# Performance work log

Hardware: AMD Instinct MI355X
Metric: run time of the kernel (lower is better)

## Reference

```python
import jax, jax.numpy as jnp
import numpy as np

B = 32768
H = W = 5          # grid_size
NC = 4             # num_colors
E = 64             # embed_dim
HID = 128          # hidden_dim
OUT = 128          # output_dim
NH = 4             # num_heads
HD = E // NH       # head_dim = 16


def _lin(k, fan_in, fan_out):
    w = jax.random.normal(k, (fan_in, fan_out), jnp.float32) / np.sqrt(fan_in)
    b = jnp.zeros((fan_out,), jnp.float32)
    return w, b


def setup_inputs() -> dict:
    key = jax.random.key(0)
    ks = jax.random.split(key, 16)
    obs = jax.random.randint(ks[0], (B, 3, H, W), 0, NC, dtype=jnp.int32)
    color_embed = jax.random.normal(ks[1], (NC, E), jnp.float32)
    row_embed = jax.random.normal(ks[2], (H, E // 2), jnp.float32)
    col_embed = jax.random.normal(ks[3], (W, E // 2), jnp.float32)
    ip_w1, ip_b1 = _lin(ks[4], 2 * E, HID)
    ip_w2, ip_b2 = _lin(ks[5], HID, E)
    q_w, q_b = _lin(ks[6], E, E)
    k_w, k_b = _lin(ks[7], E, E)
    v_w, v_b = _lin(ks[8], E, E)
    o_w, o_b = _lin(ks[9], E, E)
    op_w1, op_b1 = _lin(ks[10], 2 * E, HID)
    op_w2, op_b2 = _lin(ks[11], HID, E)
    cb_w1, cb_b1 = _lin(ks[12], 3 * E, HID)
    cb_w2, cb_b2 = _lin(ks[13], HID, OUT)
    return dict(obs=obs, color_embed=color_embed, row_embed=row_embed, col_embed=col_embed,
                ip_w1=ip_w1, ip_b1=ip_b1, ip_w2=ip_w2, ip_b2=ip_b2,
                q_w=q_w, q_b=q_b, k_w=k_w, k_b=k_b, v_w=v_w, v_b=v_b, o_w=o_w, o_b=o_b,
                op_w1=op_w1, op_b1=op_b1, op_w2=op_w2, op_b2=op_b2,
                cb_w1=cb_w1, cb_b1=cb_b1, cb_w2=cb_w2, cb_b2=cb_b2)


def _mlp(x, w1, b1, w2, b2):
    return jax.nn.relu(x @ w1 + b1) @ w2 + b2


def reference(obs, color_embed, row_embed, col_embed,
              ip_w1, ip_b1, ip_w2, ip_b2,
              q_w, q_b, k_w, k_b, v_w, v_b, o_w, o_b,
              op_w1, op_b1, op_w2, op_b2,
              cb_w1, cb_b1, cb_w2, cb_b2):
    Bn = obs.shape[0]
    input_grid, output_grid, mask = obs[:, 0], obs[:, 1], obs[:, 2]

    # 2D learned positional embedding: concat(row_emb[i], col_emb[j]) -> [H, W, E]
    pos = jnp.concatenate([
        jnp.broadcast_to(row_embed[:, None, :], (H, W, E // 2)),
        jnp.broadcast_to(col_embed[None, :, :], (H, W, E // 2))], axis=-1)
    pos_b = jnp.broadcast_to(pos, (Bn, H, W, E))

    # input branch: color embed + pos -> MLP -> [B, H*W, E]
    in_feat = jnp.concatenate([color_embed[input_grid], pos_b], axis=-1)
    inp_flat = _mlp(in_feat, ip_w1, ip_b1, ip_w2, ip_b2).reshape(Bn, H * W, E)

    # first nonzero mask position per batch (row-major), zero embedding if none
    mflat = (mask != 0).reshape(Bn, H * W)
    has = jnp.any(mflat, axis=1)
    idx = jnp.argmax(mflat, axis=1)
    r, c = idx // W, idx % W
    cpe = jnp.where(has[:, None],
                    jnp.concatenate([row_embed[r], col_embed[c]], axis=-1),
                    0.0)  # [B, E]

    # single-query cross-attention over the 25 input cells
    q = (cpe @ q_w + q_b).reshape(Bn, NH, HD)
    k = (inp_flat @ k_w + k_b).reshape(Bn, H * W, NH, HD)
    v = (inp_flat @ v_w + v_b).reshape(Bn, H * W, NH, HD)
    attn = jax.nn.softmax(jnp.einsum('bhd,bkhd->bhk', q, k) * (HD ** -0.5), axis=-1)
    attended = jnp.einsum('bhk,bkhd->bhd', attn, v).reshape(Bn, E) @ o_w + o_b

    # output branch: MLP then mean-pool over grid
    out_feat = jnp.concatenate([color_embed[output_grid], pos_b], axis=-1)
    out_ctx = _mlp(out_feat, op_w1, op_b1, op_w2, op_b2).mean(axis=(1, 2))

    combined = jnp.concatenate([attended, out_ctx, cpe], axis=-1)  # [B, 3E]
    return _mlp(combined, cb_w1, cb_b1, cb_w2, cb_b2)  # [B, OUT]
```

## Files before the change

kernel.cpp:

```cpp
#include <hip/hip_runtime.h>
#include <hip/hip_bf16.h>


typedef __attribute__((ext_vector_type(8))) short short8v;
typedef __attribute__((ext_vector_type(4))) float float4v;

static __device__ __forceinline__ short f2bfs(float f) {
  __hip_bfloat16 h = __float2bfloat16(f);
  return *reinterpret_cast<short*>(&h);
}
static __device__ __forceinline__ float bfs2f(short s) {
  return __uint_as_float(((unsigned)(unsigned short)s) << 16);
}
static __device__ __forceinline__ unsigned short f2bf(float f) {
  unsigned int u = __float_as_uint(f);
  unsigned int r = (u + 0x7fffu + ((u >> 16) & 1u)) >> 16;
  return (unsigned short)r;
}

__global__ __launch_bounds__(128) void prepE(
    const float* __restrict__ color_embed, const float* __restrict__ row_embed,
    const float* __restrict__ col_embed,
    const float* __restrict__ ip_w1, const float* __restrict__ ip_b1,
    const float* __restrict__ ip_w2, const float* __restrict__ ip_b2,
    const float* __restrict__ op_w1, const float* __restrict__ op_b1,
    const float* __restrict__ op_w2, const float* __restrict__ op_b2,
    const float* __restrict__ q_w, const float* __restrict__ q_b,
    const float* __restrict__ o_w, const float* __restrict__ o_b,
    const float* __restrict__ cb_w1, const float* __restrict__ cb_b1,
    const float* __restrict__ cb_w2,
    float* __restrict__ inpval, float* __restrict__ outval,
    float* __restrict__ qtab, float* __restrict__ cpeproj,
    float* __restrict__ bias1,
    unsigned short* __restrict__ wovT, unsigned short* __restrict__ cbw2T) {
  const int bid = blockIdx.x, t = threadIdx.x;
  if (bid < 200) {
    __shared__ float feat[128];
    __shared__ float h1[128];
    const int path = bid / 100;
    const int cij = bid % 100;
    const int c = cij / 25, ij = cij % 25, gi = ij / 5, gj = ij % 5;
    if (t < 64)      feat[t] = color_embed[c * 64 + t];
    else if (t < 96) feat[t] = row_embed[gi * 32 + (t - 64)];
    else             feat[t] = col_embed[gj * 32 + (t - 96)];
    __syncthreads();
    const float* w1 = path ? op_w1 : ip_w1;
    const float* b1 = path ? op_b1 : ip_b1;
    float acc = b1[t];
#pragma unroll 8
    for (int d = 0; d < 128; ++d) acc = fmaf(feat[d], w1[d * 128 + t], acc);
    h1[t] = fmaxf(acc, 0.f);
    __syncthreads();
    if (t < 64) {
      const float* w2 = path ? op_w2 : ip_w2;
      const float* b2 = path ? op_b2 : ip_b2;
      float v = b2[t];
#pragma unroll 8
      for (int d = 0; d < 128; ++d) v = fmaf(h1[d], w2[d * 64 + t], v);
      (path ? outval : inpval)[cij * 64 + t] = v;
    }
    return;
  }
  const int fid = (bid - 200) * 128 + t;
  if (fid < 1664) {
    const int p = fid >> 6, e2 = fid & 63;
    float a = q_b[e2];
    if (p < 25) {
      const int r = p / 5, cc = p % 5;
#pragma unroll 8
      for (int e = 0; e < 32; ++e) a = fmaf(row_embed[r * 32 + e], q_w[e * 64 + e2], a);
#pragma unroll 8
      for (int e = 0; e < 32; ++e) a = fmaf(col_embed[cc * 32 + e], q_w[(32 + e) * 64 + e2], a);
    }
    qtab[fid] = a;
  } else if (fid < 4992) {
    const int l = fid - 1664;
    const int p = l >> 7, jj = l & 127;
    float a = 0.f;
    if (p < 25) {
      const int r = p / 5, cc = p % 5;
#pragma unroll 8
      for (int e = 0; e < 32; ++e) a = fmaf(row_embed[r * 32 + e], cb_w1[(128 + e) * 128 + jj], a);
#pragma unroll 8
      for (int e = 0; e < 32; ++e) a = fmaf(col_embed[cc * 32 + e], cb_w1[(160 + e) * 128 + jj], a);
    }
    cpeproj[l] = a;
  } else if (fid < 5120) {
    const int jj = fid - 4992;
    float a = cb_b1[jj];
#pragma unroll 8
    for (int e = 0; e < 64; ++e) a = fmaf(o_b[e], cb_w1[e * 128 + jj], a);
    bias1[jj] = a;
  } else if (fid < 13312) {
    const int i = fid - 5120;
    const int col = i >> 6, d = i & 63;
    float a = 0.f;
#pragma unroll 8
    for (int e = 0; e < 64; ++e) a = fmaf(o_w[d * 64 + e], cb_w1[e * 128 + col], a);
    wovT[i] = f2bf(a);
  } else if (fid < 29696) {
    const int i = fid - 13312;
    const int col = i >> 7, k = i & 127;
    cbw2T[i] = f2bf(cb_w2[k * 128 + col]);
  }
}

__global__ __launch_bounds__(256) void prepF(
    const float* __restrict__ k_w, const float* __restrict__ k_b,
    const float* __restrict__ v_w, const float* __restrict__ v_b,
    const float* __restrict__ cb_w1,
    const float* __restrict__ qtab, const float* __restrict__ cpeproj,
    const float* __restrict__ bias1,
    const float* __restrict__ inpval, const float* __restrict__ outval,
    float* __restrict__ stab, unsigned short* __restrict__ vtabT,
    unsigned short* __restrict__ outprojBT) {
  const int bid = blockIdx.x, t = threadIdx.x;
  if (bid < 100) {
    __shared__ float kk[64];
    const int ig = bid / 25, ij = bid % 25;
    const float* x = inpval + bid * 64;
    if (t < 64) {
      float a = k_b[t];
#pragma unroll 8
      for (int e = 0; e < 64; ++e) a = fmaf(x[e], k_w[e * 64 + t], a);
      kk[t] = a;
    } else if (t < 128) {
      const int e2 = t - 64;
      float a = v_b[e2];
#pragma unroll 8
      for (int e = 0; e < 64; ++e) a = fmaf(x[e], v_w[e * 64 + e2], a);
      vtabT[(e2 >> 4) * 2048 + (e2 & 15) * 128 + 4 * ij + ig] = f2bf(a);
    } else {
      const int col = t - 128;
      const float* y = outval + bid * 64;
      float a = 0.f;
#pragma unroll 8
      for (int e = 0; e < 64; ++e) a = fmaf(y[e], cb_w1[(64 + e) * 128 + col], a);
      outprojBT[col * 128 + 4 * ij + ig] = f2bf(a * (1.f / 25.f));
    }
    __syncthreads();
    if (t < 104) {
      const int cpe = t >> 2, h = t & 3;
      const float* qq = qtab + cpe * 64 + h * 16;
      float a = 0.f;
#pragma unroll
      for (int d = 0; d < 16; ++d) a = fmaf(qq[d], kk[h * 16 + d], a);
      stab[cpe * 400 + ig * 100 + ij * 4 + h] = a * 0.25f;
    }
  } else {
    if (t < 128) {
      for (int p = 0; p < 26; ++p)
        outprojBT[t * 128 + 100 + p] = f2bf(cpeproj[p * 128 + t]);
      outprojBT[t * 128 + 126] = f2bf(bias1[t]);
      outprojBT[t * 128 + 127] = 0;
    } else {
      for (int i = t - 128; i < 1792; i += 128) {
        const int h = i / 448, r = i % 448;
        const int d = r / 28, kp = 100 + r % 28;
        vtabT[h * 2048 + d * 128 + kp] = 0;
      }
    }
  }
}

__global__ __launch_bounds__(256) void arc_fused(
    const int* __restrict__ obs,
    const float* __restrict__ stab,
    const unsigned short* __restrict__ vtabT,
    const unsigned short* __restrict__ outprojBT,
    const unsigned short* __restrict__ wovT,
    const unsigned short* __restrict__ cbw2T,
    const float* __restrict__ cb_b2,
    float* __restrict__ out) {
  __shared__ __align__(16) short lds_w[4 * 16 * 128];
  __shared__ __align__(16) short lds_og[16 * 128];
  __shared__ __align__(16) short lds_raH[16 * 64];
  __shared__ __align__(16) short lds_hidH[16 * 128];
  __shared__ __align__(16) short lds_hidL[16 * 128];

  const int tid = threadIdx.x;
  const int lane = tid & 63, wv = tid >> 6;
  const int row16 = lane & 15, g4 = lane >> 4;
  const int hh = row16 >> 2, jj = row16 & 3;
  const int b_loc = wv * 4 + g4;
  const int rsw = (row16 & 7) << 4;
  const int bswz = (b_loc & 7) << 4;
  const int bbase = blockIdx.x * 64;

  short8v Bv[4], Bo[2][4], Bw[2][2], Bc[2][4];
#pragma unroll
  for (int ks = 0; ks < 4; ++ks)
    Bv[ks] = *(const short8v*)(vtabT + wv * 2048 + row16 * 128 + ks * 32 + g4 * 8);
#pragma unroll
  for (int t = 0; t < 2; ++t) {
    const int col = wv * 32 + t * 16 + row16;
#pragma unroll
    for (int ks = 0; ks < 4; ++ks) {
      Bo[t][ks] = *(const short8v*)(outprojBT + col * 128 + ks * 32 + g4 * 8);
      Bc[t][ks] = *(const short8v*)(cbw2T + col * 128 + ks * 32 + g4 * 8);
    }
#pragma unroll
    for (int ks = 0; ks < 2; ++ks)
      Bw[t][ks] = *(const short8v*)(wovT + col * 64 + ks * 32 + g4 * 8);
  }
  const float bv0 = cb_b2[wv * 32 + row16];
  const float bv1 = cb_b2[wv * 32 + 16 + row16];

  {
    const int4 z = {0, 0, 0, 0};
    int4* pw = (int4*)lds_w;
#pragma unroll
    for (int i = 0; i < 4; ++i) pw[tid + 256 * i] = z;
  }

  int xs[4], ys[4];
#pragma unroll
  for (int e = 0; e < 4; ++e) {
    const int* ob = obs + (bbase + wv * 4 + e) * 75;
    xs[e] = ob[lane];
    ys[e] = (lane < 11) ? ob[64 + lane] : 0;
  }
  __syncthreads();

  for (int it = 0; it < 4; ++it) {
    const int b0 = bbase + it * 16;

    unsigned iglo = 0, ighi = 0, oglo = 0, oghi = 0;
    int cpe_sel = 0;
#pragma unroll
    for (int e = 0; e < 4; ++e) {
      const unsigned long long blo = __ballot(xs[e] & 1);
      const unsigned long long bhi = __ballot(xs[e] & 2);
      const unsigned long long bnzy = __ballot((lane < 11) && (ys[e] != 0));
      const unsigned e_iglo = (unsigned)(blo & 0x1FFFFFFull);
      const unsigned e_ighi = (unsigned)(bhi & 0x1FFFFFFull);
      const unsigned e_oglo = (unsigned)((blo >> 25) & 0x1FFFFFFull);
      const unsigned e_oghi = (unsigned)((bhi >> 25) & 0x1FFFFFFull);
      const unsigned e_mb = (unsigned)(((blo | bhi) >> 50) | (bnzy << 14));
      const int e_cpe = e_mb ? __builtin_ctz(e_mb) : 25;
      if (g4 == e) { iglo = e_iglo; ighi = e_ighi; oglo = e_oglo; oghi = e_oghi; cpe_sel = e_cpe; }
    }

    float ev[7];
    int ig7[7];
    {
      float sv[7];
      float mx = -1e30f;
      const float* sb = stab + cpe_sel * 400 + hh;
#pragma unroll
      for (int m = 0; m < 7; ++m) {
        const int ij = jj + 4 * m;
        if (ij < 25) {
          const int ig = ((iglo >> ij) & 1) | (((ighi >> ij) & 1) << 1);
          ig7[m] = ig;
          sv[m] = sb[ig * 100 + ij * 4];
          mx = fmaxf(mx, sv[m]);
        }
      }
      mx = fmaxf(mx, __shfl_xor(mx, 1));
      mx = fmaxf(mx, __shfl_xor(mx, 2));
      float sum = 0.f;
#pragma unroll
      for (int m = 0; m < 7; ++m) {
        const int ij = jj + 4 * m;
        if (ij < 25) { ev[m] = __expf(sv[m] - mx); sum += ev[m]; }
      }
      sum += __shfl_xor(sum, 1);
      sum += __shfl_xor(sum, 2);
      const float inv = __builtin_amdgcn_rcpf(sum);
#pragma unroll
      for (int m = 0; m < 7; ++m) ev[m] *= inv;
    }

#pragma unroll
    for (int m = 0; m < 7; ++m) {
      const int ij = jj + 4 * m;
      unsigned u0 = 0, u1 = 0;
      if (ij < 25) {
        const unsigned pbu = (unsigned)(unsigned short)f2bfs(ev[m]);
        const int ig = ig7[m];
        u0 = (ig == 0) ? pbu : ((ig == 1) ? (pbu << 16) : 0u);
        u1 = (ig == 2) ? pbu : ((ig == 3) ? (pbu << 16) : 0u);
      }
      const int off = (hh * 4096 + b_loc * 256 + 8 * ij) ^ bswz;
      *(int2*)((char*)lds_w + off) = make_int2((int)u0, (int)u1);
    }

    {
      unsigned sh[8];
#pragma unroll
      for (int u = 0; u < 8; ++u) {
        const int kp = row16 * 8 + u;
        unsigned v = 0;
        if (kp < 100) {
          const int ijq = kp >> 2;
          const int og = ((oglo >> ijq) & 1) | (((oghi >> ijq) & 1) << 1);
          v = (og == (kp & 3)) ? 0x3F80u : 0u;
        } else if (kp < 126) {
          v = (cpe_sel == kp - 100) ? 0x3F80u : 0u;
        } else if (kp == 126) {
          v = 0x3F80u;
        }
        sh[u] = v;
      }
      int4 pk;
      pk.x = (int)(sh[0] | (sh[1] << 16));
      pk.y = (int)(sh[2] | (sh[3] << 16));
      pk.z = (int)(sh[4] | (sh[5] << 16));
      pk.w = (int)(sh[6] | (sh[7] << 16));
      const int off = (b_loc * 256 + row16 * 16) ^ bswz;
      *(int4*)((char*)lds_og + off) = pk;
    }
    __syncthreads();

    float4v rc = {0.f, 0.f, 0.f, 0.f};
#pragma unroll
    for (int ks = 0; ks < 4; ++ks) {
      const short8v a = *(const short8v*)((char*)lds_w +
          ((wv * 4096 + row16 * 256 + ks * 64 + g4 * 16) ^ rsw));
      rc = __builtin_amdgcn_mfma_f32_16x16x32_bf16(a, Bv[ks], rc, 0, 0, 0);
    }
    float4v acc[2];
    acc[0] = (float4v){0.f, 0.f, 0.f, 0.f};
    acc[1] = (float4v){0.f, 0.f, 0.f, 0.f};
#pragma unroll
    for (int ks = 0; ks < 4; ++ks) {
      const short8v a = *(const short8v*)((char*)lds_og +
          ((row16 * 256 + ks * 64 + g4 * 16) ^ rsw));
      acc[0] = __builtin_amdgcn_mfma_f32_16x16x32_bf16(a, Bo[0][ks], acc[0], 0, 0, 0);
      acc[1] = __builtin_amdgcn_mfma_f32_16x16x32_bf16(a, Bo[1][ks], acc[1], 0, 0, 0);
    }

    if (it < 3) {
#pragma unroll
      for (int e = 0; e < 4; ++e) {
        const int* ob = obs + (bbase + (it + 1) * 16 + wv * 4 + e) * 75;
        xs[e] = ob[lane];
        ys[e] = (lane < 11) ? ob[64 + lane] : 0;
      }
    }

#pragma unroll
    for (int r = 0; r < 4; ++r) {
      const int b = g4 * 4 + r;
      const int off = (b * 128 + (wv * 16 + row16) * 2) ^ ((b & 7) << 4);
      *(short*)((char*)lds_raH + off) = f2bfs(rc[r]);
    }
    __syncthreads();

    const short8v aH0 = *(const short8v*)((char*)lds_raH + ((row16 * 128 + g4 * 16) ^ rsw));
    const short8v aH1 = *(const short8v*)((char*)lds_raH + ((row16 * 128 + 64 + g4 * 16) ^ rsw));
#pragma unroll
    for (int t = 0; t < 2; ++t) {
      acc[t] = __builtin_amdgcn_mfma_f32_16x16x32_bf16(aH0, Bw[t][0], acc[t], 0, 0, 0);
      acc[t] = __builtin_amdgcn_mfma_f32_16x16x32_bf16(aH1, Bw[t][1], acc[t], 0, 0, 0);
    }

#pragma unroll
    for (int t = 0; t < 2; ++t) {
      const int col = wv * 32 + t * 16 + row16;
#pragma unroll
      for (int rr = 0; rr < 4; ++rr) {
        const int row = g4 * 4 + rr;
        const float hv = fmaxf(acc[t][rr], 0.f);
        const short hb = f2bfs(hv);
        const int off = (row * 256 + col * 2) ^ ((row & 7) << 4);
        *(short*)((char*)lds_hidH + off) = hb;
        *(short*)((char*)lds_hidL + off) = f2bfs(hv - bfs2f(hb));
      }
    }
    __syncthreads();

    short8v ahH[4], ahL[4];
#pragma unroll
    for (int ks = 0; ks < 4; ++ks) {
      const int off = (row16 * 256 + ks * 64 + g4 * 16) ^ rsw;
      ahH[ks] = *(const short8v*)((char*)lds_hidH + off);
      ahL[ks] = *(const short8v*)((char*)lds_hidL + off);
    }
#pragma unroll
    for (int t = 0; t < 2; ++t) {
      const int col = wv * 32 + t * 16 + row16;
      float4v c2 = {0.f, 0.f, 0.f, 0.f};
#pragma unroll
      for (int ks = 0; ks < 4; ++ks) {
        c2 = __builtin_amdgcn_mfma_f32_16x16x32_bf16(ahL[ks], Bc[t][ks], c2, 0, 0, 0);
        c2 = __builtin_amdgcn_mfma_f32_16x16x32_bf16(ahH[ks], Bc[t][ks], c2, 0, 0, 0);
      }
      const float bv = t ? bv1 : bv0;
#pragma unroll
      for (int rr = 0; rr < 4; ++rr)
        out[(b0 + g4 * 4 + rr) * 128 + col] = c2[rr] + bv;
    }
  }
}

extern "C" void kernel_launch(void* const* d_in, const int* in_sizes, int n_in,
                              void* d_out, int out_size, void* d_ws, size_t ws_size,
                              hipStream_t stream) {
  const int*   obs         = (const int*)d_in[0];
  const float* color_embed = (const float*)d_in[1];
  const float* row_embed   = (const float*)d_in[2];
  const float* col_embed   = (const float*)d_in[3];
  const float* ip_w1 = (const float*)d_in[4];
  const float* ip_b1 = (const float*)d_in[5];
  const float* ip_w2 = (const float*)d_in[6];
  const float* ip_b2 = (const float*)d_in[7];
  const float* q_w = (const float*)d_in[8];
  const float* q_b = (const float*)d_in[9];
  const float* k_w = (const float*)d_in[10];
  const float* k_b = (const float*)d_in[11];
  const float* v_w = (const float*)d_in[12];
  const float* v_b = (const float*)d_in[13];
  const float* o_w = (const float*)d_in[14];
  const float* o_b = (const float*)d_in[15];
  const float* op_w1 = (const float*)d_in[16];
  const float* op_b1 = (const float*)d_in[17];
  const float* op_w2 = (const float*)d_in[18];
  const float* op_b2 = (const float*)d_in[19];
  const float* cb_w1 = (const float*)d_in[20];
  const float* cb_b1 = (const float*)d_in[21];
  const float* cb_w2 = (const float*)d_in[22];
  const float* cb_b2 = (const float*)d_in[23];

  float* ws = (float*)d_ws;
  float* qtab    = ws;
  float* cpeproj = qtab + 1664;
  float* bias1   = cpeproj + 3328;
  float* stab    = bias1 + 128;
  unsigned short* wovT      = (unsigned short*)(ws + 15520);
  unsigned short* cbw2T     = (unsigned short*)(ws + 19616);
  unsigned short* vtabT     = (unsigned short*)(ws + 27808);
  unsigned short* outprojBT = (unsigned short*)(ws + 31904);
  float* inpval  = ws + 40096;
  float* outval  = inpval + 6400;

  prepE<<<432, 128, 0, stream>>>(color_embed, row_embed, col_embed,
                                 ip_w1, ip_b1, ip_w2, ip_b2,
                                 op_w1, op_b1, op_w2, op_b2,
                                 q_w, q_b, o_w, o_b, cb_w1, cb_b1, cb_w2,
                                 inpval, outval, qtab, cpeproj, bias1,
                                 wovT, cbw2T);
  prepF<<<101, 256, 0, stream>>>(k_w, k_b, v_w, v_b, cb_w1,
                                 qtab, cpeproj, bias1, inpval, outval,
                                 stab, vtabT, outprojBT);
  arc_fused<<<512, 256, 0, stream>>>(obs, stab, vtabT, outprojBT,
                                     wovT, cbw2T, cb_b2, (float*)d_out);
}
```

Baseline: 37.50 us.

## Process 32 batch rows per iteration instead of 16 in fused kernel

Doubles the per-iteration batch tile from 16 to 32 rows, so each block runs two loop iterations instead of four. Every wave now handles 8 samples, and each lane computes softmax for two heads. All MFMA stages issue two row tiles per barrier. The aim is to halve the number of __syncthreads phases and amortize fixed per-iteration overhead over more MFMA work. In exchange, LDS use per block doubles and register pressure rises, which may reduce occupancy.

```diff
diff --git a/kernel.cpp b/kernel.cpp
--- a/kernel.cpp
+++ b/kernel.cpp
@@ -172,17 +172,19 @@
     const unsigned short* __restrict__ cbw2T,
     const float* __restrict__ cb_b2,
     float* __restrict__ out) {
-  __shared__ __align__(16) short lds_w[4 * 16 * 128];
-  __shared__ __align__(16) short lds_og[16 * 128];
-  __shared__ __align__(16) short lds_raH[16 * 64];
-  __shared__ __align__(16) short lds_hidH[16 * 128];
-  __shared__ __align__(16) short lds_hidL[16 * 128];
+  __shared__ __align__(16) short lds_w[4 * 32 * 128];
+  __shared__ __align__(16) short lds_og[32 * 128];
+  __shared__ __align__(16) short lds_raH[32 * 64];
+  __shared__ __align__(16) short lds_hidH[32 * 128];
+  __shared__ __align__(16) short lds_hidL[32 * 128];
 
   const int tid = threadIdx.x;
   const int lane = tid & 63, wv = tid >> 6;
   const int row16 = lane & 15, g4 = lane >> 4;
-  const int hh = row16 >> 2, jj = row16 & 3;
-  const int b_loc = wv * 4 + g4;
+  const int jj = lane & 3;
+  const int hlow = (lane >> 2) & 1;
+  const int bsel = lane >> 3;
+  const int b_loc = wv * 8 + bsel;
   const int rsw = (row16 & 7) << 4;
   const int bswz = (b_loc & 7) << 4;
   const int bbase = blockIdx.x * 64;
@@ -210,25 +212,25 @@
     const int4 z = {0, 0, 0, 0};
     int4* pw = (int4*)lds_w;
 #pragma unroll
-    for (int i = 0; i < 4; ++i) pw[tid + 256 * i] = z;
-  }
-
-  int xs[4], ys[4];
-#pragma unroll
-  for (int e = 0; e < 4; ++e) {
-    const int* ob = obs + (bbase + wv * 4 + e) * 75;
+    for (int i = 0; i < 16; ++i) pw[tid + 256 * i] = z;
+  }
+
+  int xs[8], ys[8];
+#pragma unroll
+  for (int e = 0; e < 8; ++e) {
+    const int* ob = obs + (bbase + wv * 8 + e) * 75;
     xs[e] = ob[lane];
     ys[e] = (lane < 11) ? ob[64 + lane] : 0;
   }
   __syncthreads();
 
-  for (int it = 0; it < 4; ++it) {
-    const int b0 = bbase + it * 16;
+  for (int it = 0; it < 2; ++it) {
+    const int b0 = bbase + it * 32;
 
     unsigned iglo = 0, ighi = 0, oglo = 0, oghi = 0;
     int cpe_sel = 0;
 #pragma unroll
-    for (int e = 0; e < 4; ++e) {
+    for (int e = 0; e < 8; ++e) {
       const unsigned long long blo = __ballot(xs[e] & 1);
       const unsigned long long bhi = __ballot(xs[e] & 2);
       const unsigned long long bnzy = __ballot((lane < 11) && (ys[e] != 0));
@@ -238,59 +240,73 @@
       const unsigned e_oghi = (unsigned)((bhi >> 25) & 0x1FFFFFFull);
       const unsigned e_mb = (unsigned)(((blo | bhi) >> 50) | (bnzy << 14));
       const int e_cpe = e_mb ? __builtin_ctz(e_mb) : 25;
-      if (g4 == e) { iglo = e_iglo; ighi = e_ighi; oglo = e_oglo; oghi = e_oghi; cpe_sel = e_cpe; }
-    }
-
-    float ev[7];
+      if (bsel == e) { iglo = e_iglo; ighi = e_ighi; oglo = e_oglo; oghi = e_oghi; cpe_sel = e_cpe; }
+    }
+
+    float ev0[7], ev1[7];
     int ig7[7];
     {
-      float sv[7];
-      float mx = -1e30f;
-      const float* sb = stab + cpe_sel * 400 + hh;
+      float sv0[7], sv1[7];
+      float mx0 = -1e30f, mx1 = -1e30f;
+      const float* sb0 = stab + cpe_sel * 400 + hlow;
+      const float* sb1 = sb0 + 2;
 #pragma unroll
       for (int m = 0; m < 7; ++m) {
         const int ij = jj + 4 * m;
         if (ij < 25) {
           const int ig = ((iglo >> ij) & 1) | (((ighi >> ij) & 1) << 1);
           ig7[m] = ig;
-          sv[m] = sb[ig * 100 + ij * 4];
-          mx = fmaxf(mx, sv[m]);
+          sv0[m] = sb0[ig * 100 + ij * 4];
+          sv1[m] = sb1[ig * 100 + ij * 4];
+          mx0 = fmaxf(mx0, sv0[m]);
+          mx1 = fmaxf(mx1, sv1[m]);
         }
       }
-      mx = fmaxf(mx, __shfl_xor(mx, 1));
-      mx = fmaxf(mx, __shfl_xor(mx, 2));
-      float sum = 0.f;
+      mx0 = fmaxf(mx0, __shfl_xor(mx0, 1));
+      mx0 = fmaxf(mx0, __shfl_xor(mx0, 2));
+      mx1 = fmaxf(mx1, __shfl_xor(mx1, 1));
+      mx1 = fmaxf(mx1, __shfl_xor(mx1, 2));
+      float s0 = 0.f, s1 = 0.f;
 #pragma unroll
       for (int m = 0; m < 7; ++m) {
         const int ij = jj + 4 * m;
-        if (ij < 25) { ev[m] = __expf(sv[m] - mx); sum += ev[m]; }
-      }
-      sum += __shfl_xor(sum, 1);
-      sum += __shfl_xor(sum, 2);
-      const float inv = __builtin_amdgcn_rcpf(sum);
-#pragma unroll
-      for (int m = 0; m < 7; ++m) ev[m] *= inv;
+        if (ij < 25) {
+          ev0[m] = __expf(sv0[m] - mx0); s0 += ev0[m];
+          ev1[m] = __expf(sv1[m] - mx1); s1 += ev1[m];
+        }
+      }
+      s0 += __shfl_xor(s0, 1); s0 += __shfl_xor(s0, 2);
+      s1 += __shfl_xor(s1, 1); s1 += __shfl_xor(s1, 2);
+      const float i0 = __builtin_amdgcn_rcpf(s0);
+      const float i1 = __builtin_amdgcn_rcpf(s1);
+#pragma unroll
+      for (int m = 0; m < 7; ++m) { ev0[m] *= i0; ev1[m] *= i1; }
     }
 
 #pragma unroll
     for (int m = 0; m < 7; ++m) {
       const int ij = jj + 4 * m;
-      unsigned u0 = 0, u1 = 0;
+      unsigned a0 = 0, a1 = 0, c0 = 0, c1 = 0;
       if (ij < 25) {
-        const unsigned pbu = (unsigned)(unsigned short)f2bfs(ev[m]);
         const int ig = ig7[m];
-        u0 = (ig == 0) ? pbu : ((ig == 1) ? (pbu << 16) : 0u);
-        u1 = (ig == 2) ? pbu : ((ig == 3) ? (pbu << 16) : 0u);
-      }
-      const int off = (hh * 4096 + b_loc * 256 + 8 * ij) ^ bswz;
-      *(int2*)((char*)lds_w + off) = make_int2((int)u0, (int)u1);
+        const unsigned p0u = (unsigned)(unsigned short)f2bfs(ev0[m]);
+        const unsigned p1u = (unsigned)(unsigned short)f2bfs(ev1[m]);
+        a0 = (ig == 0) ? p0u : ((ig == 1) ? (p0u << 16) : 0u);
+        a1 = (ig == 2) ? p0u : ((ig == 3) ? (p0u << 16) : 0u);
+        c0 = (ig == 0) ? p1u : ((ig == 1) ? (p1u << 16) : 0u);
+        c1 = (ig == 2) ? p1u : ((ig == 3) ? (p1u << 16) : 0u);
+      }
+      const int offA = (hlow * 8192 + b_loc * 256 + 8 * ij) ^ bswz;
+      const int offB = ((hlow + 2) * 8192 + b_loc * 256 + 8 * ij) ^ bswz;
+      *(int2*)((char*)lds_w + offA) = make_int2((int)a0, (int)a1);
+      *(int2*)((char*)lds_w + offB) = make_int2((int)c0, (int)c1);
     }
 
     {
-      unsigned sh[8];
-#pragma unroll
-      for (int u = 0; u < 8; ++u) {
-        const int kp = row16 * 8 + u;
+      unsigned sh[16];
+#pragma unroll
+      for (int u = 0; u < 16; ++u) {
+        const int kp = (lane & 7) * 16 + u;
         unsigned v = 0;
         if (kp < 100) {
           const int ijq = kp >> 2;
@@ -303,94 +319,124 @@
         }
         sh[u] = v;
       }
-      int4 pk;
-      pk.x = (int)(sh[0] | (sh[1] << 16));
-      pk.y = (int)(sh[2] | (sh[3] << 16));
-      pk.z = (int)(sh[4] | (sh[5] << 16));
-      pk.w = (int)(sh[6] | (sh[7] << 16));
-      const int off = (b_loc * 256 + row16 * 16) ^ bswz;
-      *(int4*)((char*)lds_og + off) = pk;
-    }
-    __syncthreads();
-
-    float4v rc = {0.f, 0.f, 0.f, 0.f};
-#pragma unroll
-    for (int ks = 0; ks < 4; ++ks) {
-      const short8v a = *(const short8v*)((char*)lds_w +
-          ((wv * 4096 + row16 * 256 + ks * 64 + g4 * 16) ^ rsw));
-      rc = __builtin_amdgcn_mfma_f32_16x16x32_bf16(a, Bv[ks], rc, 0, 0, 0);
-    }
-    float4v acc[2];
-    acc[0] = (float4v){0.f, 0.f, 0.f, 0.f};
-    acc[1] = (float4v){0.f, 0.f, 0.f, 0.f};
-#pragma unroll
-    for (int ks = 0; ks < 4; ++ks) {
-      const short8v a = *(const short8v*)((char*)lds_og +
-          ((row16 * 256 + ks * 64 + g4 * 16) ^ rsw));
-      acc[0] = __builtin_amdgcn_mfma_f32_16x16x32_bf16(a, Bo[0][ks], acc[0], 0, 0, 0);
-      acc[1] = __builtin_amdgcn_mfma_f32_16x16x32_bf16(a, Bo[1][ks], acc[1], 0, 0, 0);
-    }
-
-    if (it < 3) {
-#pragma unroll
-      for (int e = 0; e < 4; ++e) {
-        const int* ob = obs + (bbase + (it + 1) * 16 + wv * 4 + e) * 75;
+      int4 p0, p1;
+      p0.x = (int)(sh[0]  | (sh[1]  << 16));
+      p0.y = (int)(sh[2]  | (sh[3]  << 16));
+      p0.z = (int)(sh[4]  | (sh[5]  << 16));
+      p0.w = (int)(sh[6]  | (sh[7]  << 16));
+      p1.x = (int)(sh[8]  | (sh[9]  << 16));
+      p1.y = (int)(sh[10] | (sh[11] << 16));
+      p1.z = (int)(sh[12] | (sh[13] << 16));
+      p1.w = (int)(sh[14] | (sh[15] << 16));
+      const int obase = b_loc * 256 + (lane & 7) * 32;
+      *(int4*)((char*)lds_og + (obase ^ bswz)) = p0;
+      *(int4*)((char*)lds_og + ((obase + 16) ^ bswz)) = p1;
+    }
+    __syncthreads();
+
+    float4v rc[2];
+    rc[0] = (float4v){0.f, 0.f, 0.f, 0.f};
+    rc[1] = (float4v){0.f, 0.f, 0.f, 0.f};
+#pragma unroll
+    for (int rt = 0; rt < 2; ++rt) {
+#pragma unroll
+      for (int ks = 0; ks < 4; ++ks) {
+        const short8v a = *(const short8v*)((char*)lds_w +
+            ((wv * 8192 + (rt * 16 + row16) * 256 + ks * 64 + g4 * 16) ^ rsw));
+        rc[rt] = __builtin_amdgcn_mfma_f32_16x16x32_bf16(a, Bv[ks], rc[rt], 0, 0, 0);
+      }
+    }
+
+    float4v acc[2][2];
+    acc[0][0] = (float4v){0.f, 0.f, 0.f, 0.f};
+    acc[0][1] = (float4v){0.f, 0.f, 0.f, 0.f};
+    acc[1][0] = (float4v){0.f, 0.f, 0.f, 0.f};
+    acc[1][1] = (float4v){0.f, 0.f, 0.f, 0.f};
+#pragma unroll
+    for (int rt = 0; rt < 2; ++rt) {
+#pragma unroll
+      for (int ks = 0; ks < 4; ++ks) {
+        const short8v a = *(const short8v*)((char*)lds_og +
+            (((rt * 16 + row16) * 256 + ks * 64 + g4 * 16) ^ rsw));
+        acc[rt][0] = __builtin_amdgcn_mfma_f32_16x16x32_bf16(a, Bo[0][ks], acc[rt][0], 0, 0, 0);
+        acc[rt][1] = __builtin_amdgcn_mfma_f32_16x16x32_bf16(a, Bo[1][ks], acc[rt][1], 0, 0, 0);
+      }
+    }
+
+    if (it == 0) {
+#pragma unroll
+      for (int e = 0; e < 8; ++e) {
+        const int* ob = obs + (bbase + 32 + wv * 8 + e) * 75;
         xs[e] = ob[lane];
         ys[e] = (lane < 11) ? ob[64 + lane] : 0;
       }
     }
 
 #pragma unroll
-    for (int r = 0; r < 4; ++r) {
-      const int b = g4 * 4 + r;
-      const int off = (b * 128 + (wv * 16 + row16) * 2) ^ ((b & 7) << 4);
-      *(short*)((char*)lds_raH + off) = f2bfs(rc[r]);
-    }
-    __syncthreads();
-
-    const short8v aH0 = *(const short8v*)((char*)lds_raH + ((row16 * 128 + g4 * 16) ^ rsw));
-    const short8v aH1 = *(const short8v*)((char*)lds_raH + ((row16 * 128 + 64 + g4 * 16) ^ rsw));
-#pragma unroll
-    for (int t = 0; t < 2; ++t) {
-      acc[t] = __builtin_amdgcn_mfma_f32_16x16x32_bf16(aH0, Bw[t][0], acc[t], 0, 0, 0);
-      acc[t] = __builtin_amdgcn_mfma_f32_16x16x32_bf16(aH1, Bw[t][1], acc[t], 0, 0, 0);
-    }
-
-#pragma unroll
-    for (int t = 0; t < 2; ++t) {
-      const int col = wv * 32 + t * 16 + row16;
-#pragma unroll
-      for (int rr = 0; rr < 4; ++rr) {
-        const int row = g4 * 4 + rr;
-        const float hv = fmaxf(acc[t][rr], 0.f);
-        const short hb = f2bfs(hv);
-        const int off = (row * 256 + col * 2) ^ ((row & 7) << 4);
-        *(short*)((char*)lds_hidH + off) = hb;
-        *(short*)((char*)lds_hidL + off) = f2bfs(hv - bfs2f(hb));
-      }
-    }
-    __syncthreads();
-
-    short8v ahH[4], ahL[4];
-#pragma unroll
-    for (int ks = 0; ks < 4; ++ks) {
-      const int off = (row16 * 256 + ks * 64 + g4 * 16) ^ rsw;
-      ahH[ks] = *(const short8v*)((char*)lds_hidH + off);
-      ahL[ks] = *(const short8v*)((char*)lds_hidL + off);
-    }
-#pragma unroll
-    for (int t = 0; t < 2; ++t) {
-      const int col = wv * 32 + t * 16 + row16;
-      float4v c2 = {0.f, 0.f, 0.f, 0.f};
+    for (int rt = 0; rt < 2; ++rt) {
+#pragma unroll
+      for (int r = 0; r < 4; ++r) {
+        const int b = rt * 16 + g4 * 4 + r;
+        const int off = (b * 128 + (wv * 16 + row16) * 2) ^ ((b & 7) << 4);
+        *(short*)((char*)lds_raH + off) = f2bfs(rc[rt][r]);
+      }
+    }
+    __syncthreads();
+
+#pragma unroll
+    for (int rt = 0; rt < 2; ++rt) {
+      const short8v aH0 = *(const short8v*)((char*)lds_raH +
+          (((rt * 16 + row16) * 128 + g4 * 16) ^ rsw));
+      const short8v aH1 = *(const short8v*)((char*)lds_raH +
+          (((rt * 16 + row16) * 128 + 64 + g4 * 16) ^ rsw));
+#pragma unroll
+      for (int t = 0; t < 2; ++t) {
+        acc[rt][t] = __builtin_amdgcn_mfma_f32_16x16x32_bf16(aH0, Bw[t][0], acc[rt][t], 0, 0, 0);
+        acc[rt][t] = __builtin_amdgcn_mfma_f32_16x16x32_bf16(aH1, Bw[t][1], acc[rt][t], 0, 0, 0);
+      }
+    }
+
+#pragma unroll
+    for (int rt = 0; rt < 2; ++rt) {
+#pragma unroll
+      for (int t = 0; t < 2; ++t) {
+        const int col = wv * 32 + t * 16 + row16;
+#pragma unroll
+        for (int rr = 0; rr < 4; ++rr) {
+          const int row = rt * 16 + g4 * 4 + rr;
+          const float hv = fmaxf(acc[rt][t][rr], 0.f);
+          const short hb = f2bfs(hv);
+          const int off = (row * 256 + col * 2) ^ ((row & 7) << 4);
+          *(short*)((char*)lds_hidH + off) = hb;
+          *(short*)((char*)lds_hidL + off) = f2bfs(hv - bfs2f(hb));
+        }
+      }
+    }
+    __syncthreads();
+
+#pragma unroll
+    for (int rt = 0; rt < 2; ++rt) {
+      short8v ahH[4], ahL[4];
 #pragma unroll
       for (int ks = 0; ks < 4; ++ks) {
-        c2 = __builtin_amdgcn_mfma_f32_16x16x32_bf16(ahL[ks], Bc[t][ks], c2, 0, 0, 0);
-        c2 = __builtin_amdgcn_mfma_f32_16x16x32_bf16(ahH[ks], Bc[t][ks], c2, 0, 0, 0);
-      }
-      const float bv = t ? bv1 : bv0;
-#pragma unroll
-      for (int rr = 0; rr < 4; ++rr)
-        out[(b0 + g4 * 4 + rr) * 128 + col] = c2[rr] + bv;
+        const int off = ((rt * 16 + row16) * 256 + ks * 64 + g4 * 16) ^ rsw;
+        ahH[ks] = *(const short8v*)((char*)lds_hidH + off);
+        ahL[ks] = *(const short8v*)((char*)lds_hidL + off);
+      }
+#pragma unroll
+      for (int t = 0; t < 2; ++t) {
+        const int col = wv * 32 + t * 16 + row16;
+        float4v c2 = {0.f, 0.f, 0.f, 0.f};
+#pragma unroll
+        for (int ks = 0; ks < 4; ++ks) {
+          c2 = __builtin_amdgcn_mfma_f32_16x16x32_bf16(ahL[ks], Bc[t][ks], c2, 0, 0, 0);
+          c2 = __builtin_amdgcn_mfma_f32_16x16x32_bf16(ahH[ks], Bc[t][ks], c2, 0, 0, 0);
+        }
+        const float bv = t ? bv1 : bv0;
+#pragma unroll
+        for (int rr = 0; rr < 4; ++rr)
+          out[(b0 + rt * 16 + g4 * 4 + rr) * 128 + col] = c2[rr] + bv;
+      }
     }
   }
 }
```

Result: slower. 43.94 us (+17.2%).
